# Kernel optimization log

Hardware: AMD Instinct MI355X
Metric: run time of the kernel (lower is better)

The kernel has to match this reference:

```python
import jax, jax.numpy as jnp
import numpy as np

B, H, W, C = 16, 32, 32, 512
HEADS, DHEAD = 8, 64  # head * channel == C
GROUPS, EPS = 32, 1e-5


def setup_inputs() -> dict:
    key = jax.random.key(0)
    ks = jax.random.split(key, 6)
    return {
        "x": jax.random.normal(ks[0], (B, H, W, C), jnp.float32),
        "gn_gamma": jnp.ones((C,), jnp.float32),
        "gn_beta": jnp.zeros((C,), jnp.float32),
        "wq": jax.random.normal(ks[1], (C, HEADS * DHEAD), jnp.float32) * 0.02,
        "wk": jax.random.normal(ks[2], (C, HEADS * DHEAD), jnp.float32) * 0.02,
        "wv": jax.random.normal(ks[3], (C, HEADS * DHEAD), jnp.float32) * 0.02,
        "conv_w": jax.random.normal(ks[4], (3, 3, HEADS * DHEAD, C), jnp.float32) * 0.02,
        "conv_b": jnp.zeros((C,), jnp.float32),
    }


def _group_norm(x, gamma, beta):
    b, h, w, c = x.shape
    xg = x.reshape(b, h, w, GROUPS, c // GROUPS)
    mean = jnp.mean(xg, axis=(1, 2, 4), keepdims=True)
    var = jnp.var(xg, axis=(1, 2, 4), keepdims=True)
    xn = (xg - mean) * jax.lax.rsqrt(var + EPS)
    return xn.reshape(b, h, w, c) * gamma + beta


def reference(x, gn_gamma, gn_beta, wq, wk, wv, conv_w, conv_b):
    xn = _group_norm(x, gn_gamma, gn_beta)          # [B,H,W,C]
    t = xn.reshape(B, H * W, C)                      # tokens [B,S,C]
    q = (t @ wq).reshape(B, H * W, HEADS, DHEAD)
    k = (t @ wk).reshape(B, H * W, HEADS, DHEAD)
    v = (t @ wv).reshape(B, H * W, HEADS, DHEAD)
    scale = 1.0 / jnp.sqrt(jnp.asarray(DHEAD, q.dtype))
    scores = jnp.einsum("bqhd,bkhd->bhqk", q, k) * scale  # [B,HEADS,S,S]
    weights = jax.nn.softmax(scores, axis=-1)
    out = jnp.einsum("bhqk,bkhd->bqhd", weights, v)       # [B,S,HEADS,DHEAD]
    out = out.reshape(B, H, W, HEADS * DHEAD)
    y = jax.lax.conv_general_dilated(
        out, conv_w, window_strides=(1, 1), padding=((1, 1), (1, 1)),
        dimension_numbers=("NHWC", "HWIO", "NHWC")) + conv_b
    return y + x
```

## Files before the change

### kernel.cpp

```cpp
#include <hip/hip_runtime.h>
#include <hip/hip_bf16.h>

#define Bn 16
#define Cc 512
#define Ss 1024
#define HEADS 8
#define DHEAD 64
#define GROUPS 32
#define CPG 16
#define EPSv 1e-5f
#define Mtok (Bn*Ss)
#define QKVS 1536
#define QKS 1024
#define PROW 34
#define PIMG (PROW*PROW)

typedef __hip_bfloat16 bf16;
typedef __attribute__((ext_vector_type(8))) short short8;
typedef __attribute__((ext_vector_type(4))) float f32x4;

union U4 { uint4 u; bf16 h[8]; };
union B4 { ushort4 u; bf16 h[4]; };

__device__ __forceinline__ void stage16(const bf16* g, bf16* l) {
    __builtin_amdgcn_global_load_lds((const __attribute__((address_space(1))) void*)g,
                                     (__attribute__((address_space(3))) void*)l,
                                     16, 0, 0);
}

__device__ __forceinline__ unsigned int pkbf(float a, float b) {
    union { __hip_bfloat16 h; unsigned short u; } ua, ub;
    ua.h = __float2bfloat16(a); ub.h = __float2bfloat16(b);
    return ((unsigned int)ub.u << 16) | ua.u;
}

__device__ __forceinline__ void swz_decode(int F, int& r, int& c) {
    int line = F >> 3, pos = F & 7;
    int u = pos ^ (line & 7);
    r = (line << 1) | (u >> 2);
    c = u & 3;
}
__device__ __forceinline__ int swz_off(int r, int q) {
    return (r >> 1) * 64 + (((((r & 1) << 2) + q) ^ ((r >> 1) & 7)) << 3);
}

__global__ __launch_bounds__(256) void wtrans(const float* __restrict__ src,
                                              bf16* __restrict__ dst) {
    size_t off = (size_t)blockIdx.y * 262144;
    int t = blockIdx.x * 256 + threadIdx.x;
    int n = t & 511, k8 = (t >> 9) * 8;
    const float* s = src + off + (size_t)k8 * 512 + n;
    U4 o;
#pragma unroll
    for (int j = 0; j < 8; j++) o.h[j] = __float2bfloat16(s[(size_t)j * 512]);
    *(uint4*)(dst + off + (size_t)n * 512 + k8) = o.u;
}

__global__ __launch_bounds__(256) void gn_stats(const float* __restrict__ x,
                                                float* __restrict__ stats) {
    int bg = blockIdx.x;
    int b = bg >> 5, g = bg & 31;
    int tid = threadIdx.x;
    const size_t base = (size_t)b * Ss * Cc + g * CPG;
    float sum = 0.f, sq = 0.f;
    for (int i = tid; i < 4096; i += 256) {
        int s = i >> 2, c4 = (i & 3) * 4;
        float4 t = *(const float4*)(x + base + (size_t)s * Cc + c4);
        sum += t.x + t.y + t.z + t.w;
        sq  += t.x * t.x + t.y * t.y + t.z * t.z + t.w * t.w;
    }
    __shared__ float s1[4], s2[4];
#pragma unroll
    for (int off = 32; off > 0; off >>= 1) {
        sum += __shfl_down(sum, off);
        sq  += __shfl_down(sq,  off);
    }
    if ((tid & 63) == 0) { s1[tid >> 6] = sum; s2[tid >> 6] = sq; }
    __syncthreads();
    if (tid == 0) {
        float S = s1[0] + s1[1] + s1[2] + s1[3];
        float Q = s2[0] + s2[1] + s2[2] + s2[3];
        float mean = S * (1.f / 16384.f);
        float var  = Q * (1.f / 16384.f) - mean * mean;
        stats[bg * 2 + 0] = mean;
        stats[bg * 2 + 1] = rsqrtf(var + EPSv);
    }
}

__global__ __launch_bounds__(256) void gn_apply(const float* __restrict__ x,
                                                const float* __restrict__ stats,
                                                const float* __restrict__ gamma,
                                                const float* __restrict__ beta,
                                                bf16* __restrict__ xn) {
    size_t i = (size_t)blockIdx.x * 256 + threadIdx.x;
    size_t e = i * 4;
    int c0 = (int)(e & (Cc - 1));
    int token = (int)(e >> 9);
    int b = token >> 10;
    int g = c0 >> 4;
    float mean = stats[(b * 32 + g) * 2 + 0];
    float rstd = stats[(b * 32 + g) * 2 + 1];
    float4 t  = *(const float4*)(x + e);
    float4 gm = *(const float4*)(gamma + c0);
    float4 bt = *(const float4*)(beta + c0);
    B4 o;
    o.h[0] = __float2bfloat16((t.x - mean) * rstd * gm.x + bt.x);
    o.h[1] = __float2bfloat16((t.y - mean) * rstd * gm.y + bt.y);
    o.h[2] = __float2bfloat16((t.z - mean) * rstd * gm.z + bt.z);
    o.h[3] = __float2bfloat16((t.w - mean) * rstd * gm.w + bt.w);
    *(ushort4*)(xn + e) = o.u;
}

__global__ __launch_bounds__(256) void zero_pad(bf16* __restrict__ Pad) {
    int idx = blockIdx.x * 256 + threadIdx.x;
    int b = idx / (132 * 64);
    int rem = idx - b * 132 * 64;
    int t = rem >> 6, seg = rem & 63;
    int r, c;
    if (t < 34)      { r = 0;  c = t; }
    else if (t < 68) { r = 33; c = t - 34; }
    else { int u = t - 68; r = 1 + (u >> 1); c = (u & 1) * 33; }
    uint4 z = {0u, 0u, 0u, 0u};
    *(uint4*)(Pad + ((size_t)b * PIMG + r * PROW + c) * Cc + seg * 8) = z;
}

__global__ __launch_bounds__(256) void gemm_qkv(const bf16* __restrict__ A,
                                                const bf16* __restrict__ Wt,
                                                bf16* __restrict__ C,
                                                bf16* __restrict__ vT) {
    __shared__ __align__(16) bf16 As[128][32];
    __shared__ __align__(16) bf16 Bs[128][32];
    int tid = threadIdx.x;
    int wave = tid >> 6, lane = tid & 63;
    int l15 = lane & 15, quad = lane >> 4;
    int wm = wave >> 1, wn = wave & 1;
    int m0 = blockIdx.y * 128, n0 = blockIdx.x * 128;
    int lr = lane >> 2, kseg = (lane & 3) * 8;
    int ar0 = wave * 32 + lr;

    const bf16* ga = A  + (size_t)(m0 + ar0) * Cc + kseg;
    const bf16* gb = Wt + (size_t)(n0 + ar0) * Cc + kseg;
    bf16* la0 = &As[wave * 32][0];
    bf16* la1 = &As[wave * 32 + 16][0];
    bf16* lb0 = &Bs[wave * 32][0];
    bf16* lb1 = &Bs[wave * 32 + 16][0];

    f32x4 acc[4][4] = {};
    for (int k0 = 0; k0 < 512; k0 += 32) {
        __syncthreads();
        stage16(ga + k0,                  la0);
        stage16(ga + k0 + (size_t)16 * Cc, la1);
        stage16(gb + k0,                  lb0);
        stage16(gb + k0 + (size_t)16 * Cc, lb1);
        __syncthreads();
        short8 af[4], bfv[4];
#pragma unroll
        for (int mt = 0; mt < 4; mt++) af[mt]  = *(const short8*)&As[wm * 64 + mt * 16 + l15][quad * 8];
#pragma unroll
        for (int nt = 0; nt < 4; nt++) bfv[nt] = *(const short8*)&Bs[wn * 64 + nt * 16 + l15][quad * 8];
#pragma unroll
        for (int mt = 0; mt < 4; mt++)
#pragma unroll
            for (int nt = 0; nt < 4; nt++)
                acc[mt][nt] = __builtin_amdgcn_mfma_f32_16x16x32_bf16(af[mt], bfv[nt], acc[mt][nt], 0, 0, 0);
    }

    if (n0 < 1024) {
#pragma unroll
        for (int mt = 0; mt < 4; mt++)
#pragma unroll
            for (int r = 0; r < 4; r++) {
                size_t row = (size_t)(m0 + wm * 64 + mt * 16 + quad * 4 + r) * QKS + n0 + wn * 64 + l15;
#pragma unroll
                for (int nt = 0; nt < 4; nt++)
                    C[row + nt * 16] = __float2bfloat16(acc[mt][nt][r]);
            }
    } else {
        int hh = ((n0 - 1024) >> 6) + wn;
        int bq = m0 >> 10;
        int tok0 = (m0 & 1023) + wm * 64;
#pragma unroll
        for (int nt = 0; nt < 4; nt++) {
            int d = nt * 16 + l15;
            bf16* drow = vT + (size_t)(hh * 64 + d) * 16384 + bq * 1024 + tok0;
#pragma unroll
            for (int mt = 0; mt < 4; mt++) {
                B4 o;
#pragma unroll
                for (int r = 0; r < 4; r++) o.h[r] = __float2bfloat16(acc[mt][nt][r]);
                *(ushort4*)(drow + mt * 16 + quad * 4) = o.u;
            }
        }
    }
}

__global__ __launch_bounds__(256) void attention_mfma(const bf16* __restrict__ QK,
                                                      const bf16* __restrict__ vT,
                                                      bf16* __restrict__ Pad) {
    int blk = blockIdx.x;
    int qt = blk & 7;
    int bh = blk >> 3;
    int h = bh & (HEADS - 1), b = bh >> 3;
    int tid = threadIdx.x;
    int wave = tid >> 6, lane = tid & 63;
    int l15 = lane & 15, quad = lane >> 4;

    __shared__ __align__(16) bf16 KT[2][4096];
    __shared__ __align__(16) bf16 VTs[2][4096];

    const size_t base = (size_t)b * Ss * QKS + h * DHEAD;
    const bf16* kbase = QK + base + 512;

    int q0 = qt * 128 + wave * 32;
    const bf16* qrow = QK + base + (size_t)(q0 + l15) * QKS + quad * 8;
    short8 qfA0 = *(const short8*)(qrow);
    short8 qfA1 = *(const short8*)(qrow + 32);
    short8 qfB0 = *(const short8*)(qrow + 16 * QKS);
    short8 qfB1 = *(const short8*)(qrow + 16 * QKS + 32);

    int r1 = tid >> 3,         f1 = (tid & 7) ^ (r1 & 7);
    int r2 = (tid + 256) >> 3, f2 = ((tid + 256) & 7) ^ (r2 & 7);
    const bf16* gk1 = kbase + (size_t)r1 * QKS + f1 * 8;
    const bf16* gk2 = kbase + (size_t)r2 * QKS + f2 * 8;
    const bf16* gv1 = vT + (size_t)(h * 64 + r1) * 16384 + b * 1024 + f1 * 8;
    const bf16* gv2 = vT + (size_t)(h * 64 + r2) * 16384 + b * 1024 + f2 * 8;

    f32x4 oacc0[4] = {{0.f,0.f,0.f,0.f},{0.f,0.f,0.f,0.f},{0.f,0.f,0.f,0.f},{0.f,0.f,0.f,0.f}};
    f32x4 oacc1[4] = {{0.f,0.f,0.f,0.f},{0.f,0.f,0.f,0.f},{0.f,0.f,0.f,0.f},{0.f,0.f,0.f,0.f}};
    float lsum0 = 0.f, lsum1 = 0.f;
    const f32x4 zero4 = {0.f, 0.f, 0.f, 0.f};
    int srcA = ((quad & 1) * 2) * 16 + l15;
    int srcB = srcA + 16;
    bool hiq = (quad >= 2);
    int sw = l15 & 7;

    auto stage = [&](int c0, int p) {
        stage16(gk1 + (size_t)c0 * QKS, &KT[p][wave * 512]);
        stage16(gk2 + (size_t)c0 * QKS, &KT[p][2048 + wave * 512]);
        stage16(gv1 + c0,               &VTs[p][wave * 512]);
        stage16(gv2 + c0,               &VTs[p][2048 + wave * 512]);
    };

    stage(0, 0);
    for (int it = 0; it < 16; ++it) {
        int p = it & 1;
        if (it + 1 < 16) {
            stage((it + 1) * 64, p ^ 1);
            asm volatile("s_waitcnt vmcnt(4)" ::: "memory");
        } else {
            asm volatile("s_waitcnt vmcnt(0)" ::: "memory");
        }
        __builtin_amdgcn_s_barrier();
        __builtin_amdgcn_sched_barrier(0);

        unsigned int pk0[4][2], pk1[4][2];
        __builtin_amdgcn_s_setprio(1);
#pragma unroll
        for (int kb = 0; kb < 4; kb++) {
            const bf16* kr = &KT[p][(kb * 16 + l15) * 64];
            short8 kf0 = *(const short8*)(kr + ((quad ^ sw) * 8));
            short8 kf1 = *(const short8*)(kr + (((4 + quad) ^ sw) * 8));
            f32x4 s0 = __builtin_amdgcn_mfma_f32_16x16x32_bf16(kf0, qfA0, zero4, 0, 0, 0);
            s0 = __builtin_amdgcn_mfma_f32_16x16x32_bf16(kf1, qfA1, s0, 0, 0, 0);
            f32x4 s1 = __builtin_amdgcn_mfma_f32_16x16x32_bf16(kf0, qfB0, zero4, 0, 0, 0);
            s1 = __builtin_amdgcn_mfma_f32_16x16x32_bf16(kf1, qfB1, s1, 0, 0, 0);
            float a0 = __expf(s0[0] * 0.125f);
            float a1 = __expf(s0[1] * 0.125f);
            float a2 = __expf(s0[2] * 0.125f);
            float a3 = __expf(s0[3] * 0.125f);
            lsum0 += (a0 + a1) + (a2 + a3);
            pk0[kb][0] = pkbf(a0, a1);
            pk0[kb][1] = pkbf(a2, a3);
            float b0 = __expf(s1[0] * 0.125f);
            float b1 = __expf(s1[1] * 0.125f);
            float b2 = __expf(s1[2] * 0.125f);
            float b3 = __expf(s1[3] * 0.125f);
            lsum1 += (b0 + b1) + (b2 + b3);
            pk1[kb][0] = pkbf(b0, b1);
            pk1[kb][1] = pkbf(b2, b3);
        }
        __builtin_amdgcn_s_setprio(0);

        union { short8 s8; unsigned int u[4]; } PT00, PT01, PT10, PT11;
        {
            unsigned int A0 = __shfl((int)pk0[0][0], srcA), A1 = __shfl((int)pk0[0][1], srcA);
            unsigned int A2 = __shfl((int)pk0[1][0], srcA), A3 = __shfl((int)pk0[1][1], srcA);
            unsigned int B0 = __shfl((int)pk0[0][0], srcB), B1 = __shfl((int)pk0[0][1], srcB);
            unsigned int B2 = __shfl((int)pk0[1][0], srcB), B3 = __shfl((int)pk0[1][1], srcB);
            PT00.u[0] = hiq ? A2 : A0;  PT00.u[1] = hiq ? A3 : A1;
            PT00.u[2] = hiq ? B2 : B0;  PT00.u[3] = hiq ? B3 : B1;
            unsigned int C0 = __shfl((int)pk0[2][0], srcA), C1 = __shfl((int)pk0[2][1], srcA);
            unsigned int C2 = __shfl((int)pk0[3][0], srcA), C3 = __shfl((int)pk0[3][1], srcA);
            unsigned int D0 = __shfl((int)pk0[2][0], srcB), D1 = __shfl((int)pk0[2][1], srcB);
            unsigned int D2 = __shfl((int)pk0[3][0], srcB), D3 = __shfl((int)pk0[3][1], srcB);
            PT01.u[0] = hiq ? C2 : C0;  PT01.u[1] = hiq ? C3 : C1;
            PT01.u[2] = hiq ? D2 : D0;  PT01.u[3] = hiq ? D3 : D1;
        }
        {
            unsigned int A0 = __shfl((int)pk1[0][0], srcA), A1 = __shfl((int)pk1[0][1], srcA);
            unsigned int A2 = __shfl((int)pk1[1][0], srcA), A3 = __shfl((int)pk1[1][1], srcA);
            unsigned int B0 = __shfl((int)pk1[0][0], srcB), B1 = __shfl((int)pk1[0][1], srcB);
            unsigned int B2 = __shfl((int)pk1[1][0], srcB), B3 = __shfl((int)pk1[1][1], srcB);
            PT10.u[0] = hiq ? A2 : A0;  PT10.u[1] = hiq ? A3 : A1;
            PT10.u[2] = hiq ? B2 : B0;  PT10.u[3] = hiq ? B3 : B1;
            unsigned int C0 = __shfl((int)pk1[2][0], srcA), C1 = __shfl((int)pk1[2][1], srcA);
            unsigned int C2 = __shfl((int)pk1[3][0], srcA), C3 = __shfl((int)pk1[3][1], srcA);
            unsigned int D0 = __shfl((int)pk1[2][0], srcB), D1 = __shfl((int)pk1[2][1], srcB);
            unsigned int D2 = __shfl((int)pk1[3][0], srcB), D3 = __shfl((int)pk1[3][1], srcB);
            PT11.u[0] = hiq ? C2 : C0;  PT11.u[1] = hiq ? C3 : C1;
            PT11.u[2] = hiq ? D2 : D0;  PT11.u[3] = hiq ? D3 : D1;
        }

        __builtin_amdgcn_s_setprio(1);
#pragma unroll
        for (int dt = 0; dt < 4; dt++) {
            const bf16* vr = &VTs[p][(dt * 16 + l15) * 64];
            short8 vf0 = *(const short8*)(vr + ((quad ^ sw) * 8));
            short8 vf1 = *(const short8*)(vr + (((4 + quad) ^ sw) * 8));
            oacc0[dt] = __builtin_amdgcn_mfma_f32_16x16x32_bf16(vf0, PT00.s8, oacc0[dt], 0, 0, 0);
            oacc0[dt] = __builtin_amdgcn_mfma_f32_16x16x32_bf16(vf1, PT01.s8, oacc0[dt], 0, 0, 0);
            oacc1[dt] = __builtin_amdgcn_mfma_f32_16x16x32_bf16(vf0, PT10.s8, oacc1[dt], 0, 0, 0);
            oacc1[dt] = __builtin_amdgcn_mfma_f32_16x16x32_bf16(vf1, PT11.s8, oacc1[dt], 0, 0, 0);
        }
        __builtin_amdgcn_s_setprio(0);

        __builtin_amdgcn_sched_barrier(0);
        __builtin_amdgcn_s_barrier();
        __builtin_amdgcn_sched_barrier(0);
    }

    lsum0 += __shfl_xor(lsum0, 16);
    lsum0 += __shfl_xor(lsum0, 32);
    lsum1 += __shfl_xor(lsum1, 16);
    lsum1 += __shfl_xor(lsum1, 32);
    float inv0 = 1.f / lsum0;
    float inv1 = 1.f / lsum1;

    {
        int s = q0 + l15;
        size_t rowoff = ((size_t)(b * PROW + (s >> 5) + 1) * PROW + (s & 31) + 1) * Cc + h * DHEAD;
#pragma unroll
        for (int dt = 0; dt < 4; dt++) {
            B4 o;
#pragma unroll
            for (int r = 0; r < 4; r++) o.h[r] = __float2bfloat16(oacc0[dt][r] * inv0);
            *(ushort4*)(Pad + rowoff + dt * 16 + quad * 4) = o.u;
        }
    }
    {
        int s = q0 + 16 + l15;
        size_t rowoff = ((size_t)(b * PROW + (s >> 5) + 1) * PROW + (s & 31) + 1) * Cc + h * DHEAD;
#pragma unroll
        for (int dt = 0; dt < 4; dt++) {
            B4 o;
#pragma unroll
            for (int r = 0; r < 4; r++) o.h[r] = __float2bfloat16(oacc1[dt][r] * inv1);
            *(ushort4*)(Pad + rowoff + dt * 16 + quad * 4) = o.u;
        }
    }
}

__global__ __launch_bounds__(256, 2) void conv_mfma(const bf16* __restrict__ Pad,
                                                    const bf16* __restrict__ Wct,
                                                    const float* __restrict__ bias,
                                                    const float* __restrict__ xres,
                                                    float* __restrict__ out) {
    __shared__ __align__(16) bf16 As[2][136 * 32];
    __shared__ __align__(16) bf16 Bs[2][3 * 4096];

    int tid = threadIdx.x;
    int wave = tid >> 6, lane = tid & 63;
    int l15 = lane & 15, quad = lane >> 4;
    int wm = wave >> 1, wn = wave & 1;
    int m0 = blockIdx.y * 128, n0 = blockIdx.x * 128;
    int b = m0 >> 10, oh0 = (m0 & 1023) >> 5;

    int rA1, cA1, rA2, cA2, rA3, cA3;
    swz_decode(tid,              rA1, cA1);
    swz_decode(tid + 256,        rA2, cA2);
    swz_decode((tid & 31) + 512, rA3, cA3);
    int rr1 = rA1 / 34, co1 = rA1 - rr1 * 34;
    int rr2 = rA2 / 34, co2 = rA2 - rr2 * 34;
    int rr3 = rA3 / 34, co3 = rA3 - rr3 * 34;
    const size_t dyStride = (size_t)PROW * Cc;
    const bf16* pA1 = Pad + ((size_t)b * PIMG + (size_t)(oh0 + rr1) * PROW + co1) * Cc + cA1 * 8;
    const bf16* pA2 = Pad + ((size_t)b * PIMG + (size_t)(oh0 + rr2) * PROW + co2) * Cc + cA2 * 8;
    const bf16* pA3 = Pad + ((size_t)b * PIMG + (size_t)(oh0 + rr3) * PROW + co3) * Cc + cA3 * 8;

    int rB1, cB1, rB2, cB2;
    swz_decode(wave * 128 + lane,      rB1, cB1);
    swz_decode(wave * 128 + 64 + lane, rB2, cB2);
    const bf16* gw1 = Wct + (size_t)(n0 + rB1) * Cc + cB1 * 8;
    const bf16* gw2 = Wct + (size_t)(n0 + rB2) * Cc + cB2 * 8;

    int aoff[3][4], boff[4];
#pragma unroll
    for (int mt = 0; mt < 4; mt++) {
        int rbase = (wm * 2 + (mt >> 1)) * 34 + (mt & 1) * 16 + l15;
#pragma unroll
        for (int dxi = 0; dxi < 3; dxi++) aoff[dxi][mt] = swz_off(rbase + dxi, quad);
    }
#pragma unroll
    for (int nt = 0; nt < 4; nt++) boff[nt] = swz_off(wn * 64 + nt * 16 + l15, quad);

    auto stage_it = [&](int it, int p) {
        int dyi = it >> 4;
        int k0 = (it & 15) << 5;
        size_t ag = (size_t)dyi * dyStride + k0;
        stage16(pA1 + ag, &As[p][wave * 512]);
        stage16(pA2 + ag, &As[p][2048 + wave * 512]);
        if (tid < 32) stage16(pA3 + ag, &As[p][4096]);
        size_t wg = (size_t)(dyi * 3) * (Cc * Cc) + k0;
#pragma unroll
        for (int t = 0; t < 3; t++) {
            size_t tg = wg + (size_t)t * (Cc * Cc);
            stage16(gw1 + tg, &Bs[p][t * 4096 + wave * 1024]);
            stage16(gw2 + tg, &Bs[p][t * 4096 + wave * 1024 + 512]);
        }
    };

    f32x4 acc[4][4] = {};
    stage_it(0, 0);
    for (int it = 0; it < 48; ++it) {
        int p = it & 1;
        if (it + 1 < 48) {
            stage_it(it + 1, p ^ 1);
            asm volatile("s_waitcnt vmcnt(8)" ::: "memory");
        } else {
            asm volatile("s_waitcnt vmcnt(0)" ::: "memory");
        }
        __builtin_amdgcn_s_barrier();

        short8 af[3][4], bfv[3][4];
#pragma unroll
        for (int dxi = 0; dxi < 3; dxi++) {
#pragma unroll
            for (int mt = 0; mt < 4; mt++)
                af[dxi][mt] = *(const short8*)&As[p][aoff[dxi][mt]];
#pragma unroll
            for (int nt = 0; nt < 4; nt++)
                bfv[dxi][nt] = *(const short8*)&Bs[p][dxi * 4096 + boff[nt]];
        }
        asm volatile("s_waitcnt lgkmcnt(0)" ::: "memory");
        __builtin_amdgcn_sched_barrier(0);
        __builtin_amdgcn_s_barrier();

#pragma unroll
        for (int dxi = 0; dxi < 3; dxi++)
#pragma unroll
            for (int mt = 0; mt < 4; mt++)
#pragma unroll
                for (int nt = 0; nt < 4; nt++)
                    acc[mt][nt] = __builtin_amdgcn_mfma_f32_16x16x32_bf16(af[dxi][mt], bfv[dxi][nt], acc[mt][nt], 0, 0, 0);
    }

#pragma unroll
    for (int mt = 0; mt < 4; mt++)
#pragma unroll
        for (int r = 0; r < 4; r++) {
            size_t row = (size_t)(m0 + wm * 64 + mt * 16 + quad * 4 + r) * Cc + n0 + wn * 64 + l15;
#pragma unroll
            for (int nt = 0; nt < 4; nt++) {
                int n = n0 + wn * 64 + nt * 16 + l15;
                out[row + nt * 16] = acc[mt][nt][r] + bias[n] + xres[row + nt * 16];
            }
        }
}

extern "C" void kernel_launch(void* const* d_in, const int* in_sizes, int n_in,
                              void* d_out, int out_size, void* d_ws, size_t ws_size,
                              hipStream_t stream) {
    const float* x     = (const float*)d_in[0];
    const float* gamma = (const float*)d_in[1];
    const float* beta  = (const float*)d_in[2];
    const float* wq    = (const float*)d_in[3];
    const float* wk    = (const float*)d_in[4];
    const float* wv    = (const float*)d_in[5];
    const float* convw = (const float*)d_in[6];
    const float* convb = (const float*)d_in[7];
    float* out = (float*)d_out;

    char* ws = (char*)d_ws;
    bf16*  pad   = (bf16*)ws;
    float* stats = (float*)ws;
    bf16*  xn    = (bf16*)(ws + 4096);
    bf16*  wt    = (bf16*)(ws + 4096 + ((size_t)16 << 20));
    bf16*  qk    = (bf16*)(ws + ((size_t)19 << 20));
    bf16*  vt    = (bf16*)(ws + ((size_t)51 << 20));
    bf16*  wct   = (bf16*)(ws + ((size_t)67 << 20));

    wtrans<<<dim3(128, 1), 256, 0, stream>>>(wq, wt);
    wtrans<<<dim3(128, 1), 256, 0, stream>>>(wk, wt + 262144);
    wtrans<<<dim3(128, 1), 256, 0, stream>>>(wv, wt + 524288);
    wtrans<<<dim3(128, 9), 256, 0, stream>>>(convw, wct);

    gn_stats<<<dim3(Bn * GROUPS), 256, 0, stream>>>(x, stats);
    gn_apply<<<dim3(Mtok * Cc / (4 * 256)), 256, 0, stream>>>(x, stats, gamma, beta, xn);

    gemm_qkv<<<dim3(QKVS / 128, Mtok / 128), 256, 0, stream>>>(xn, wt, qk, vt);

    zero_pad<<<dim3(528), 256, 0, stream>>>(pad);
    attention_mfma<<<dim3(Bn * HEADS * (Ss / 128)), 256, 0, stream>>>(qk, vt, pad);

    conv_mfma<<<dim3(Cc / 128, Mtok / 128), 256, 0, stream>>>(pad, wct, convb, x, out);
}
```

Baseline: 319.0 us.

## Double-buffer QKV GEMM staging and interleave LDS reads with MFMA in conv

The QKV projection GEMM moves from a single LDS buffer with two __syncthreads per k-step to a double-buffered scheme. The next tile's global loads are issued before computing the current one, with vmcnt waits and setprio around the MFMA block. The conv GEMM inner loop is restructured so the third tap's LDS fragment reads overlap the first two taps' MFMAs instead of all reads preceding all math. This aims to hide global and LDS latency, at the cost of double the shared memory in the QKV kernel and tighter reliance on hand-placed wait counts.

```diff
diff --git a/kernel.cpp b/kernel.cpp
--- a/kernel.cpp
+++ b/kernel.cpp
@@ -128,8 +128,8 @@
                                                 const bf16* __restrict__ Wt,
                                                 bf16* __restrict__ C,
                                                 bf16* __restrict__ vT) {
-    __shared__ __align__(16) bf16 As[128][32];
-    __shared__ __align__(16) bf16 Bs[128][32];
+    __shared__ __align__(16) bf16 As[2][4096];
+    __shared__ __align__(16) bf16 Bs[2][4096];
     int tid = threadIdx.x;
     int wave = tid >> 6, lane = tid & 63;
     int l15 = lane & 15, quad = lane >> 4;
@@ -140,29 +140,42 @@
 
     const bf16* ga = A  + (size_t)(m0 + ar0) * Cc + kseg;
     const bf16* gb = Wt + (size_t)(n0 + ar0) * Cc + kseg;
-    bf16* la0 = &As[wave * 32][0];
-    bf16* la1 = &As[wave * 32 + 16][0];
-    bf16* lb0 = &Bs[wave * 32][0];
-    bf16* lb1 = &Bs[wave * 32 + 16][0];
+
+    auto stageg = [&](int k0, int p) {
+        stage16(ga + k0,                   &As[p][wave * 1024]);
+        stage16(ga + k0 + (size_t)16 * Cc, &As[p][wave * 1024 + 512]);
+        stage16(gb + k0,                   &Bs[p][wave * 1024]);
+        stage16(gb + k0 + (size_t)16 * Cc, &Bs[p][wave * 1024 + 512]);
+    };
 
     f32x4 acc[4][4] = {};
-    for (int k0 = 0; k0 < 512; k0 += 32) {
-        __syncthreads();
-        stage16(ga + k0,                  la0);
-        stage16(ga + k0 + (size_t)16 * Cc, la1);
-        stage16(gb + k0,                  lb0);
-        stage16(gb + k0 + (size_t)16 * Cc, lb1);
-        __syncthreads();
+    stageg(0, 0);
+    for (int it = 0; it < 16; ++it) {
+        int p = it & 1;
+        if (it + 1 < 16) {
+            stageg((it + 1) * 32, p ^ 1);
+            asm volatile("s_waitcnt vmcnt(4)" ::: "memory");
+        } else {
+            asm volatile("s_waitcnt vmcnt(0)" ::: "memory");
+        }
+        __builtin_amdgcn_s_barrier();
+
         short8 af[4], bfv[4];
 #pragma unroll
-        for (int mt = 0; mt < 4; mt++) af[mt]  = *(const short8*)&As[wm * 64 + mt * 16 + l15][quad * 8];
-#pragma unroll
-        for (int nt = 0; nt < 4; nt++) bfv[nt] = *(const short8*)&Bs[wn * 64 + nt * 16 + l15][quad * 8];
+        for (int mt = 0; mt < 4; mt++) af[mt]  = *(const short8*)&As[p][(wm * 64 + mt * 16 + l15) * 32 + quad * 8];
+#pragma unroll
+        for (int nt = 0; nt < 4; nt++) bfv[nt] = *(const short8*)&Bs[p][(wn * 64 + nt * 16 + l15) * 32 + quad * 8];
+        asm volatile("s_waitcnt lgkmcnt(0)" ::: "memory");
+        __builtin_amdgcn_sched_barrier(0);
+        __builtin_amdgcn_s_barrier();
+
+        __builtin_amdgcn_s_setprio(1);
 #pragma unroll
         for (int mt = 0; mt < 4; mt++)
 #pragma unroll
             for (int nt = 0; nt < 4; nt++)
                 acc[mt][nt] = __builtin_amdgcn_mfma_f32_16x16x32_bf16(af[mt], bfv[nt], acc[mt][nt], 0, 0, 0);
+        __builtin_amdgcn_s_setprio(0);
     }
 
     if (n0 < 1024) {
@@ -430,10 +443,11 @@
             asm volatile("s_waitcnt vmcnt(0)" ::: "memory");
         }
         __builtin_amdgcn_s_barrier();
+        __builtin_amdgcn_sched_barrier(0);
 
         short8 af[3][4], bfv[3][4];
 #pragma unroll
-        for (int dxi = 0; dxi < 3; dxi++) {
+        for (int dxi = 0; dxi < 2; dxi++) {
 #pragma unroll
             for (int mt = 0; mt < 4; mt++)
                 af[dxi][mt] = *(const short8*)&As[p][aoff[dxi][mt]];
@@ -441,17 +455,40 @@
             for (int nt = 0; nt < 4; nt++)
                 bfv[dxi][nt] = *(const short8*)&Bs[p][dxi * 4096 + boff[nt]];
         }
+        __builtin_amdgcn_sched_barrier(0);
+        __builtin_amdgcn_s_setprio(1);
+#pragma unroll
+        for (int mt = 0; mt < 4; mt++)
+#pragma unroll
+            for (int nt = 0; nt < 4; nt++)
+                acc[mt][nt] = __builtin_amdgcn_mfma_f32_16x16x32_bf16(af[0][mt], bfv[0][nt], acc[mt][nt], 0, 0, 0);
+        __builtin_amdgcn_s_setprio(0);
+        __builtin_amdgcn_sched_barrier(0);
+#pragma unroll
+        for (int mt = 0; mt < 4; mt++)
+            af[2][mt] = *(const short8*)&As[p][aoff[2][mt]];
+#pragma unroll
+        for (int nt = 0; nt < 4; nt++)
+            bfv[2][nt] = *(const short8*)&Bs[p][2 * 4096 + boff[nt]];
+        __builtin_amdgcn_sched_barrier(0);
+        __builtin_amdgcn_s_setprio(1);
+#pragma unroll
+        for (int mt = 0; mt < 4; mt++)
+#pragma unroll
+            for (int nt = 0; nt < 4; nt++)
+                acc[mt][nt] = __builtin_amdgcn_mfma_f32_16x16x32_bf16(af[1][mt], bfv[1][nt], acc[mt][nt], 0, 0, 0);
+        __builtin_amdgcn_s_setprio(0);
+        __builtin_amdgcn_sched_barrier(0);
         asm volatile("s_waitcnt lgkmcnt(0)" ::: "memory");
         __builtin_amdgcn_sched_barrier(0);
         __builtin_amdgcn_s_barrier();
-
-#pragma unroll
-        for (int dxi = 0; dxi < 3; dxi++)
-#pragma unroll
-            for (int mt = 0; mt < 4; mt++)
-#pragma unroll
-                for (int nt = 0; nt < 4; nt++)
-                    acc[mt][nt] = __builtin_amdgcn_mfma_f32_16x16x32_bf16(af[dxi][mt], bfv[dxi][nt], acc[mt][nt], 0, 0, 0);
+        __builtin_amdgcn_s_setprio(1);
+#pragma unroll
+        for (int mt = 0; mt < 4; mt++)
+#pragma unroll
+            for (int nt = 0; nt < 4; nt++)
+                acc[mt][nt] = __builtin_amdgcn_mfma_f32_16x16x32_bf16(af[2][mt], bfv[2][nt], acc[mt][nt], 0, 0, 0);
+        __builtin_amdgcn_s_setprio(0);
     }
 
 #pragma unroll
```

Measured after the change: 314.3 us. About the same (-1.5%).
